# Performance work log

Measured on AMD Instinct MI355X. Metric: run time of the kernel, lower is better.

The kernel has to match this reference:

```python
import jax, jax.numpy as jnp
import numpy as np

B, N = 8, 50000
NB, NA, NT, NI, NC = 60000, 120000, 180000, 20000, 1500000


def _term_index(key, n_terms, arity, n_atoms):
    # distinct atom indices per term (avoids degenerate zero-length vectors)
    k1, k2 = jax.random.split(key)
    base = jax.random.randint(k1, (n_terms,), 0, n_atoms)
    cols = [base]
    for a in range(arity - 1):
        off = jax.random.randint(jax.random.fold_in(k2, a), (n_terms,), 1, n_atoms)
        cols.append((base + off + a) % n_atoms)
    return jnp.stack(cols, axis=1).astype(jnp.int32)


def setup_inputs() -> dict:
    key = jax.random.key(0)
    ks = jax.random.split(key, 24)
    u = lambda k, s, lo, hi: jax.random.uniform(k, s, jnp.float32, lo, hi)
    coords = jax.random.normal(ks[0], (B, N, 3), jnp.float32) * 10.0
    return dict(
        coords=coords,
        bond_index=_term_index(ks[1], NB, 2, N),
        bond_rest_length=u(ks[2], (NB,), 1.0, 2.0),
        bond_force_constant=u(ks[3], (NB,), 200.0, 800.0),
        angle_index=_term_index(ks[4], NA, 3, N),
        angle_force_constant=u(ks[5], (NA,), 50.0, 300.0),
        angle_c0=u(ks[6], (NA,), 0.5, 2.0),
        angle_c1=u(ks[7], (NA,), -1.0, 1.0),
        angle_c2=u(ks[8], (NA,), -1.0, 1.0),
        torsion_index=_term_index(ks[9], NT, 4, N),
        torsion_force_constant=u(ks[10], (NT,), 1.0, 20.0),
        torsion_order=jax.random.randint(ks[11], (NT,), 1, 7).astype(jnp.int32),
        torsion_cos_term=jnp.where(jax.random.bernoulli(ks[12], 0.5, (NT,)), 1.0, -1.0).astype(jnp.float32),
        inversion_index=_term_index(ks[13], NI, 4, N),
        inversion_force_constant=u(ks[14], (NI,), 1.0, 40.0),
        inversion_c0=u(ks[15], (NI,), 0.5, 1.5),
        inversion_c1=u(ks[16], (NI,), -1.0, 1.0),
        inversion_c2=u(ks[17], (NI,), -1.0, 1.0),
        nonbond_index=_term_index(ks[18], NC, 2, N),
        vdw_minimum=u(ks[19], (NC,), 3.0, 4.0),
        vdw_well_depth=u(ks[20], (NC,), 0.01, 0.2),
        vdw_threshold_sq=jnp.square(u(ks[21], (NC,), 10.0, 30.0)),
    )


def _uff_energy(coords, bond_index, bond_rest_length, bond_force_constant,
                angle_index, angle_force_constant, angle_c0, angle_c1, angle_c2,
                torsion_index, torsion_force_constant, torsion_order, torsion_cos_term,
                inversion_index, inversion_force_constant, inversion_c0, inversion_c1, inversion_c2,
                nonbond_index, vdw_minimum, vdw_well_depth, vdw_threshold_sq):
    take = lambda idx: jnp.take(coords, idx, axis=1)  # (B, P, 3)

    # ---- bond stretch: 0.5 * k * (|r_ij| - r0)^2 ----
    d = take(bond_index[:, 0]) - take(bond_index[:, 1])
    dist = jnp.sqrt(jnp.sum(d * d, -1))
    e_bond = jnp.sum(0.5 * bond_force_constant * jnp.square(dist - bond_rest_length), -1)

    # ---- angle bend (general cosine expansion, order == 0 branch) ----
    p1, p2, p3 = take(angle_index[:, 0]), take(angle_index[:, 1]), take(angle_index[:, 2])
    v1, v2 = p1 - p2, p3 - p2
    dot = jnp.sum(v1 * v2, -1)
    inv = jax.lax.rsqrt(jnp.maximum(jnp.sum(v1 * v1, -1) * jnp.sum(v2 * v2, -1), 1e-24))
    ct = jnp.clip(dot * inv, -0.999999, 0.999999)
    cs = ct * ct
    ss = jnp.maximum(1.0 - cs, 1e-12)
    e_angle = jnp.sum(angle_force_constant * (angle_c0 + angle_c1 * ct + angle_c2 * (cs - ss)), -1)

    # ---- torsion: 0.5 * V * (1 - cos_term * cos(n * phi)) ----
    q1, q2, q3, q4 = (take(torsion_index[:, a]) for a in range(4))
    b1, b2, b3 = q2 - q1, q3 - q2, q4 - q3
    n1 = jnp.cross(b1, b2)
    n2 = jnp.cross(b2, b3)
    cn = jnp.sum(n1 * n2, -1) * jax.lax.rsqrt(
        jnp.maximum(jnp.sum(n1 * n1, -1) * jnp.sum(n2 * n2, -1), 1e-24))
    phi = jnp.arccos(jnp.clip(cn, -0.999999, 0.999999))
    n_f = torsion_order.astype(coords.dtype)
    e_tor = jnp.sum(0.5 * torsion_force_constant * (1.0 - torsion_cos_term * jnp.cos(n_f * phi)), -1)

    # ---- inversion (Wilson angle): K*(c0 + c1*sinY + c2*(2*sinY^2 - 1)), central atom = col 1 ----
    cA = take(inversion_index[:, 1])
    rji = take(inversion_index[:, 0]) - cA
    rjk = take(inversion_index[:, 2]) - cA
    rjl = take(inversion_index[:, 3]) - cA
    nrm = jnp.cross(rji, rjk)
    cosY = jnp.sum(nrm * rjl, -1) * jax.lax.rsqrt(
        jnp.maximum(jnp.sum(nrm * nrm, -1) * jnp.sum(rjl * rjl, -1), 1e-24))
    cosY = jnp.clip(cosY, -0.999999, 0.999999)
    sinY = jnp.sqrt(jnp.maximum(1.0 - cosY * cosY, 0.0))
    e_inv = jnp.sum(inversion_force_constant * (inversion_c0 + inversion_c1 * sinY
                                                + inversion_c2 * (2.0 * sinY * sinY - 1.0)), -1)

    # ---- vdW LJ on radius-graph candidates: D*((R/r)^12 - 2*(R/r)^6) within cutoff ----
    dnb = take(nonbond_index[:, 0]) - take(nonbond_index[:, 1])
    d2 = jnp.sum(dnb * dnb, -1)
    within = d2 <= vdw_threshold_sq  # pair selection done under no_grad in the original
    x2 = jnp.square(vdw_minimum) / jnp.maximum(d2, 1e-12)
    x6 = x2 * x2 * x2
    e_pair = vdw_well_depth * (x6 * x6 - 2.0 * x6)
    e_vdw = jnp.sum(jnp.where(within, e_pair, 0.0), -1)

    return e_bond + e_angle + e_tor + e_inv + e_vdw  # (B,)


def reference(coords, bond_index, bond_rest_length, bond_force_constant,
              angle_index, angle_force_constant, angle_c0, angle_c1, angle_c2,
              torsion_index, torsion_force_constant, torsion_order, torsion_cos_term,
              inversion_index, inversion_force_constant, inversion_c0, inversion_c1, inversion_c2,
              nonbond_index, vdw_minimum, vdw_well_depth, vdw_threshold_sq):
    return _uff_energy(coords, bond_index, bond_rest_length, bond_force_constant,
                       angle_index, angle_force_constant, angle_c0, angle_c1, angle_c2,
                       torsion_index, torsion_force_constant, torsion_order, torsion_cos_term,
                       inversion_index, inversion_force_constant, inversion_c0, inversion_c1, inversion_c2,
                       nonbond_index, vdw_minimum, vdw_well_depth, vdw_threshold_sq)
```

## Files before the change

kernel.cpp:

```cpp
#include <hip/hip_runtime.h>

#define TPB 256
#define NWAVE (TPB / 64)
#define GRID_MAIN 2048

typedef int vi2 __attribute__((ext_vector_type(2)));
typedef int vi4 __attribute__((ext_vector_type(4)));

struct SegInfo {
    int e0, e1, e2, e3, e4;
    int NB, NA, NT, NI, NC;
    int N;
};

__device__ __forceinline__ float clamp1(float x) {
    return fminf(fmaxf(x, -0.999999f), 0.999999f);
}

__device__ __forceinline__ float ntf(const float* p) { return __builtin_nontemporal_load(p); }
__device__ __forceinline__ int   nti(const int* p)   { return __builtin_nontemporal_load(p); }

template <bool USE_WS>
__device__ __forceinline__ float4 loadC(const float4* __restrict__ cw,
                                        const float* __restrict__ coords,
                                        int N, int atom, int b) {
    if (USE_WS) {
        return cw[((size_t)atom << 3) + b];
    } else {
        const float* sp = coords + ((size_t)b * N + atom) * 3;
        return make_float4(sp[0], sp[1], sp[2], 0.f);
    }
}

__global__ void __launch_bounds__(TPB) transpose_coords(const float* __restrict__ coords,
                                                        float4* __restrict__ cw,
                                                        float* __restrict__ out, int N) {
    const int a = blockIdx.x * TPB + threadIdx.x;
    if (blockIdx.x == 0 && threadIdx.x < 8) out[threadIdx.x] = 0.f;
    if (a >= N) return;
#pragma unroll
    for (int b = 0; b < 8; b++) {
        const float* sp = coords + ((size_t)b * N + a) * 3;
        cw[((size_t)a << 3) + b] = make_float4(ntf(sp), ntf(sp + 1), ntf(sp + 2), 0.f);
    }
}

template <bool USE_WS>
__global__ void __launch_bounds__(TPB) uff_kernel(
    const float* __restrict__ coords, const float4* __restrict__ cw,
    const int* __restrict__ bidx, const float* __restrict__ br0, const float* __restrict__ bk,
    const int* __restrict__ aidx, const float* __restrict__ ak,
    const float* __restrict__ ac0, const float* __restrict__ ac1, const float* __restrict__ ac2,
    const int* __restrict__ tidx, const float* __restrict__ tk,
    const int* __restrict__ tord, const float* __restrict__ tcos,
    const int* __restrict__ iidx, const float* __restrict__ ik,
    const float* __restrict__ ic0, const float* __restrict__ ic1, const float* __restrict__ ic2,
    const int* __restrict__ nidx, const float* __restrict__ vmin,
    const float* __restrict__ vdep, const float* __restrict__ vthr,
    float* __restrict__ out, SegInfo s)
{
    const int tid = threadIdx.x;
    const int N = s.N;
    const int b = tid & 7;
    const int gidx = tid >> 3;
    float acc = 0.f;

    for (int c = blockIdx.x; c < s.e4; c += gridDim.x) {
        int kind, l;
        if (c < s.e0)      { kind = 0; l = c; }
        else if (c < s.e1) { kind = 1; l = c - s.e0; }
        else if (c < s.e2) { kind = 2; l = c - s.e1; }
        else if (c < s.e3) { kind = 3; l = c - s.e2; }
        else               { kind = 4; l = c - s.e3; }
        const int t = l * 32 + gidx;

        if (kind == 0) {
            if (t < s.NB) {
                const vi2 ij = __builtin_nontemporal_load((const vi2*)bidx + t);
                const float r0 = ntf(br0 + t), k = ntf(bk + t);
                float4 ci = loadC<USE_WS>(cw, coords, N, ij.x, b);
                float4 cj = loadC<USE_WS>(cw, coords, N, ij.y, b);
                float dx = ci.x - cj.x, dy = ci.y - cj.y, dz = ci.z - cj.z;
                float dd = sqrtf(dx * dx + dy * dy + dz * dz) - r0;
                acc += 0.5f * k * dd * dd;
            }
        } else if (kind == 1) {
            if (t < s.NA) {
                const int i1 = nti(aidx + 3 * t), i2 = nti(aidx + 3 * t + 1), i3 = nti(aidx + 3 * t + 2);
                const float k = ntf(ak + t), c0 = ntf(ac0 + t), c1 = ntf(ac1 + t), c2 = ntf(ac2 + t);
                float4 P = loadC<USE_WS>(cw, coords, N, i1, b);
                float4 Q = loadC<USE_WS>(cw, coords, N, i2, b);
                float4 R = loadC<USE_WS>(cw, coords, N, i3, b);
                float ax = P.x - Q.x, ay = P.y - Q.y, az = P.z - Q.z;
                float bx = R.x - Q.x, by = R.y - Q.y, bz = R.z - Q.z;
                float dot = ax * bx + ay * by + az * bz;
                float nn = (ax * ax + ay * ay + az * az) * (bx * bx + by * by + bz * bz);
                float ct = clamp1(dot * rsqrtf(fmaxf(nn, 1e-24f)));
                float cs = ct * ct;
                float sb = fmaxf(1.f - cs, 1e-12f);
                acc += k * (c0 + c1 * ct + c2 * (cs - sb));
            }
        } else if (kind == 2) {
            if (t < s.NT) {
                const vi4 q = __builtin_nontemporal_load((const vi4*)tidx + t);
                const float V = ntf(tk + t), ctm = ntf(tcos + t);
                const int ord = nti(tord + t);
                float4 P1 = loadC<USE_WS>(cw, coords, N, q.x, b);
                float4 P2 = loadC<USE_WS>(cw, coords, N, q.y, b);
                float4 P3 = loadC<USE_WS>(cw, coords, N, q.z, b);
                float4 P4 = loadC<USE_WS>(cw, coords, N, q.w, b);
                float b1x = P2.x - P1.x, b1y = P2.y - P1.y, b1z = P2.z - P1.z;
                float b2x = P3.x - P2.x, b2y = P3.y - P2.y, b2z = P3.z - P2.z;
                float b3x = P4.x - P3.x, b3y = P4.y - P3.y, b3z = P4.z - P3.z;
                float n1x = b1y * b2z - b1z * b2y;
                float n1y = b1z * b2x - b1x * b2z;
                float n1z = b1x * b2y - b1y * b2x;
                float n2x = b2y * b3z - b2z * b3y;
                float n2y = b2z * b3x - b2x * b3z;
                float n2z = b2x * b3y - b2y * b3x;
                float dot = n1x * n2x + n1y * n2y + n1z * n2z;
                float nn = (n1x * n1x + n1y * n1y + n1z * n1z) *
                           (n2x * n2x + n2y * n2y + n2z * n2z);
                float x = clamp1(dot * rsqrtf(fmaxf(nn, 1e-24f)));
                float Tp = 1.f, Tc = x, res = x;
#pragma unroll
                for (int kk = 2; kk <= 6; kk++) {
                    float Tn = 2.f * x * Tc - Tp;
                    Tp = Tc; Tc = Tn;
                    if (ord == kk) res = Tn;
                }
                acc += 0.5f * V * (1.f - ctm * res);
            }
        } else if (kind == 3) {
            if (t < s.NI) {
                const vi4 q = __builtin_nontemporal_load((const vi4*)iidx + t);
                const float K = ntf(ik + t), c0 = ntf(ic0 + t), c1 = ntf(ic1 + t), c2 = ntf(ic2 + t);
                float4 CA = loadC<USE_WS>(cw, coords, N, q.y, b);
                float4 PI = loadC<USE_WS>(cw, coords, N, q.x, b);
                float4 PK = loadC<USE_WS>(cw, coords, N, q.z, b);
                float4 PL = loadC<USE_WS>(cw, coords, N, q.w, b);
                float jix = PI.x - CA.x, jiy = PI.y - CA.y, jiz = PI.z - CA.z;
                float jkx = PK.x - CA.x, jky = PK.y - CA.y, jkz = PK.z - CA.z;
                float lx  = PL.x - CA.x, ly  = PL.y - CA.y, lz  = PL.z - CA.z;
                float nx = jiy * jkz - jiz * jky;
                float ny = jiz * jkx - jix * jkz;
                float nz = jix * jky - jiy * jkx;
                float dot = nx * lx + ny * ly + nz * lz;
                float nn = (nx * nx + ny * ny + nz * nz) * (lx * lx + ly * ly + lz * lz);
                float cosY = clamp1(dot * rsqrtf(fmaxf(nn, 1e-24f)));
                float sinY = sqrtf(fmaxf(1.f - cosY * cosY, 0.f));
                acc += K * (c0 + c1 * sinY + c2 * (2.f * sinY * sinY - 1.f));
            }
        } else {
            if (t < s.NC) {
                const vi2 ij = __builtin_nontemporal_load((const vi2*)nidx + t);
                const float R = ntf(vmin + t), D = ntf(vdep + t), thr = ntf(vthr + t);
                float4 ci = loadC<USE_WS>(cw, coords, N, ij.x, b);
                float4 cj = loadC<USE_WS>(cw, coords, N, ij.y, b);
                float dx = ci.x - cj.x, dy = ci.y - cj.y, dz = ci.z - cj.z;
                float d2 = dx * dx + dy * dy + dz * dz;
                float x2 = (R * R) / fmaxf(d2, 1e-12f);
                float x6 = x2 * x2 * x2;
                float e = D * (x6 * x6 - 2.f * x6);
                if (d2 <= thr) acc += e;
            }
        }
    }

    float v = acc;
    v += __shfl_down(v, 8, 64);
    v += __shfl_down(v, 16, 64);
    v += __shfl_down(v, 32, 64);

    __shared__ float red[NWAVE][8];
    const int lane = tid & 63;
    const int wid = tid >> 6;
    if (lane < 8) red[wid][lane] = v;
    __syncthreads();
    if (tid < 8) {
        float ssum = 0.f;
#pragma unroll
        for (int w = 0; w < NWAVE; w++) ssum += red[w][tid];
        atomicAdd(&out[tid], ssum);
    }
}

static inline int cdiv(int a, int b) { return (a + b - 1) / b; }

extern "C" void kernel_launch(void* const* d_in, const int* in_sizes, int n_in,
                              void* d_out, int out_size, void* d_ws, size_t ws_size,
                              hipStream_t stream) {
    const int B = out_size;
    const int NB = in_sizes[2], NA = in_sizes[5], NT = in_sizes[10],
              NI = in_sizes[14], NC = in_sizes[19];
    const int N = in_sizes[0] / (3 * B);

    const float* coords = (const float*)d_in[0];
    const int*   bidx = (const int*)d_in[1];
    const float* br0  = (const float*)d_in[2];
    const float* bk   = (const float*)d_in[3];
    const int*   aidx = (const int*)d_in[4];
    const float* ak   = (const float*)d_in[5];
    const float* ac0  = (const float*)d_in[6];
    const float* ac1  = (const float*)d_in[7];
    const float* ac2  = (const float*)d_in[8];
    const int*   tidx = (const int*)d_in[9];
    const float* tk   = (const float*)d_in[10];
    const int*   tord = (const int*)d_in[11];
    const float* tcos = (const float*)d_in[12];
    const int*   iidx = (const int*)d_in[13];
    const float* ik   = (const float*)d_in[14];
    const float* ic0  = (const float*)d_in[15];
    const float* ic1  = (const float*)d_in[16];
    const float* ic2  = (const float*)d_in[17];
    const int*   nidx = (const int*)d_in[18];
    const float* vmin = (const float*)d_in[19];
    const float* vdep = (const float*)d_in[20];
    const float* vthr = (const float*)d_in[21];

    const size_t ws_need = (size_t)N * 8 * sizeof(float4);
    const bool use_ws = ws_size >= ws_need;
    float4* cw = (float4*)d_ws;

    if (use_ws) {
        transpose_coords<<<cdiv(N, TPB), TPB, 0, stream>>>(coords, cw, (float*)d_out, N);
    } else {
        hipMemsetAsync(d_out, 0, (size_t)out_size * sizeof(float), stream);
    }

    SegInfo s;
    s.NB = NB; s.NA = NA; s.NT = NT; s.NI = NI; s.NC = NC; s.N = N;
    s.e0 = cdiv(NB, 32);
    s.e1 = s.e0 + cdiv(NA, 32);
    s.e2 = s.e1 + cdiv(NT, 32);
    s.e3 = s.e2 + cdiv(NI, 32);
    s.e4 = s.e3 + cdiv(NC, 32);

    const int grid = (s.e4 < GRID_MAIN) ? s.e4 : GRID_MAIN;

    if (use_ws) {
        uff_kernel<true><<<grid, TPB, 0, stream>>>(
            coords, cw, bidx, br0, bk, aidx, ak, ac0, ac1, ac2,
            tidx, tk, tord, tcos, iidx, ik, ic0, ic1, ic2,
            nidx, vmin, vdep, vthr, (float*)d_out, s);
    } else {
        uff_kernel<false><<<grid, TPB, 0, stream>>>(
            coords, cw, bidx, br0, bk, aidx, ak, ac0, ac1, ac2,
            tidx, tk, tord, tcos, iidx, ik, ic0, ic1, ic2,
            nidx, vmin, vdep, vthr, (float*)d_out, s);
    }
}
```

Before: 199.3 us.

## Split per-term-type loops, broadcast term params via shuffle, double up LJ pairs

Replaces the single grid-stride loop with its per-chunk kind dispatch by five separate grid-stride loops, one per term type. Within each group of 8 lanes, only lane 0 now loads the term indices and parameters, and the values reach the other 7 lanes through wavefront shuffles. This removes the eightfold redundant per-batch loads of the same term data. The nonbond loop handles two pairs per lane group per iteration to expose more memory-level parallelism, at the cost of extra shuffle instructions and a serialized dependency on lane 0's load.

```diff
diff --git a/kernel.cpp b/kernel.cpp
--- a/kernel.cpp
+++ b/kernel.cpp
@@ -8,7 +8,7 @@
 typedef int vi4 __attribute__((ext_vector_type(4)));
 
 struct SegInfo {
-    int e0, e1, e2, e3, e4;
+    int cb, ca, ct, ci, cl;
     int NB, NA, NT, NI, NC;
     int N;
 };
@@ -18,7 +18,9 @@
 }
 
 __device__ __forceinline__ float ntf(const float* p) { return __builtin_nontemporal_load(p); }
-__device__ __forceinline__ int   nti(const int* p)   { return __builtin_nontemporal_load(p); }
+
+__device__ __forceinline__ float bcf(float v, int sl) { return __shfl(v, sl, 64); }
+__device__ __forceinline__ int   bci(int v, int sl)   { return __shfl(v, sl, 64); }
 
 template <bool USE_WS>
 __device__ __forceinline__ float4 loadC(const float4* __restrict__ cw,
@@ -60,110 +62,159 @@
     float* __restrict__ out, SegInfo s)
 {
     const int tid = threadIdx.x;
+    const int lane = tid & 63;
+    const int b = tid & 7;
+    const int g = tid >> 3;
+    const int sl = lane & ~7;
     const int N = s.N;
-    const int b = tid & 7;
-    const int gidx = tid >> 3;
     float acc = 0.f;
 
-    for (int c = blockIdx.x; c < s.e4; c += gridDim.x) {
-        int kind, l;
-        if (c < s.e0)      { kind = 0; l = c; }
-        else if (c < s.e1) { kind = 1; l = c - s.e0; }
-        else if (c < s.e2) { kind = 2; l = c - s.e1; }
-        else if (c < s.e3) { kind = 3; l = c - s.e2; }
-        else               { kind = 4; l = c - s.e3; }
-        const int t = l * 32 + gidx;
-
-        if (kind == 0) {
-            if (t < s.NB) {
-                const vi2 ij = __builtin_nontemporal_load((const vi2*)bidx + t);
-                const float r0 = ntf(br0 + t), k = ntf(bk + t);
-                float4 ci = loadC<USE_WS>(cw, coords, N, ij.x, b);
-                float4 cj = loadC<USE_WS>(cw, coords, N, ij.y, b);
-                float dx = ci.x - cj.x, dy = ci.y - cj.y, dz = ci.z - cj.z;
-                float dd = sqrtf(dx * dx + dy * dy + dz * dz) - r0;
-                acc += 0.5f * k * dd * dd;
-            }
-        } else if (kind == 1) {
-            if (t < s.NA) {
-                const int i1 = nti(aidx + 3 * t), i2 = nti(aidx + 3 * t + 1), i3 = nti(aidx + 3 * t + 2);
-                const float k = ntf(ak + t), c0 = ntf(ac0 + t), c1 = ntf(ac1 + t), c2 = ntf(ac2 + t);
-                float4 P = loadC<USE_WS>(cw, coords, N, i1, b);
-                float4 Q = loadC<USE_WS>(cw, coords, N, i2, b);
-                float4 R = loadC<USE_WS>(cw, coords, N, i3, b);
-                float ax = P.x - Q.x, ay = P.y - Q.y, az = P.z - Q.z;
-                float bx = R.x - Q.x, by = R.y - Q.y, bz = R.z - Q.z;
-                float dot = ax * bx + ay * by + az * bz;
-                float nn = (ax * ax + ay * ay + az * az) * (bx * bx + by * by + bz * bz);
-                float ct = clamp1(dot * rsqrtf(fmaxf(nn, 1e-24f)));
-                float cs = ct * ct;
-                float sb = fmaxf(1.f - cs, 1e-12f);
-                acc += k * (c0 + c1 * ct + c2 * (cs - sb));
-            }
-        } else if (kind == 2) {
-            if (t < s.NT) {
-                const vi4 q = __builtin_nontemporal_load((const vi4*)tidx + t);
-                const float V = ntf(tk + t), ctm = ntf(tcos + t);
-                const int ord = nti(tord + t);
-                float4 P1 = loadC<USE_WS>(cw, coords, N, q.x, b);
-                float4 P2 = loadC<USE_WS>(cw, coords, N, q.y, b);
-                float4 P3 = loadC<USE_WS>(cw, coords, N, q.z, b);
-                float4 P4 = loadC<USE_WS>(cw, coords, N, q.w, b);
-                float b1x = P2.x - P1.x, b1y = P2.y - P1.y, b1z = P2.z - P1.z;
-                float b2x = P3.x - P2.x, b2y = P3.y - P2.y, b2z = P3.z - P2.z;
-                float b3x = P4.x - P3.x, b3y = P4.y - P3.y, b3z = P4.z - P3.z;
-                float n1x = b1y * b2z - b1z * b2y;
-                float n1y = b1z * b2x - b1x * b2z;
-                float n1z = b1x * b2y - b1y * b2x;
-                float n2x = b2y * b3z - b2z * b3y;
-                float n2y = b2z * b3x - b2x * b3z;
-                float n2z = b2x * b3y - b2y * b3x;
-                float dot = n1x * n2x + n1y * n2y + n1z * n2z;
-                float nn = (n1x * n1x + n1y * n1y + n1z * n1z) *
-                           (n2x * n2x + n2y * n2y + n2z * n2z);
-                float x = clamp1(dot * rsqrtf(fmaxf(nn, 1e-24f)));
-                float Tp = 1.f, Tc = x, res = x;
+    for (int c = blockIdx.x; c < s.cb; c += gridDim.x) {
+        const int t = c * 32 + g;
+        const bool ok = t < s.NB;
+        int ijx = 0, ijy = 0; float r0 = 0.f, k = 0.f;
+        if (ok && b == 0) {
+            const vi2 ij = __builtin_nontemporal_load((const vi2*)bidx + t);
+            ijx = ij.x; ijy = ij.y; r0 = ntf(br0 + t); k = ntf(bk + t);
+        }
+        ijx = bci(ijx, sl); ijy = bci(ijy, sl); r0 = bcf(r0, sl); k = bcf(k, sl);
+        float4 ci = loadC<USE_WS>(cw, coords, N, ijx, b);
+        float4 cj = loadC<USE_WS>(cw, coords, N, ijy, b);
+        float dx = ci.x - cj.x, dy = ci.y - cj.y, dz = ci.z - cj.z;
+        float dd = sqrtf(dx * dx + dy * dy + dz * dz) - r0;
+        if (ok) acc += 0.5f * k * dd * dd;
+    }
+
+    for (int c = blockIdx.x; c < s.ca; c += gridDim.x) {
+        const int t = c * 32 + g;
+        const bool ok = t < s.NA;
+        int i1 = 0, i2 = 0, i3 = 0; float k = 0.f, c0 = 0.f, c1 = 0.f, c2 = 0.f;
+        if (ok && b == 0) {
+            i1 = aidx[3 * t]; i2 = aidx[3 * t + 1]; i3 = aidx[3 * t + 2];
+            k = ntf(ak + t); c0 = ntf(ac0 + t); c1 = ntf(ac1 + t); c2 = ntf(ac2 + t);
+        }
+        i1 = bci(i1, sl); i2 = bci(i2, sl); i3 = bci(i3, sl);
+        k = bcf(k, sl); c0 = bcf(c0, sl); c1 = bcf(c1, sl); c2 = bcf(c2, sl);
+        float4 P = loadC<USE_WS>(cw, coords, N, i1, b);
+        float4 Q = loadC<USE_WS>(cw, coords, N, i2, b);
+        float4 R = loadC<USE_WS>(cw, coords, N, i3, b);
+        float ax = P.x - Q.x, ay = P.y - Q.y, az = P.z - Q.z;
+        float bx = R.x - Q.x, by = R.y - Q.y, bz = R.z - Q.z;
+        float dot = ax * bx + ay * by + az * bz;
+        float nn = (ax * ax + ay * ay + az * az) * (bx * bx + by * by + bz * bz);
+        float ct = clamp1(dot * rsqrtf(fmaxf(nn, 1e-24f)));
+        float cs = ct * ct;
+        float sb = fmaxf(1.f - cs, 1e-12f);
+        if (ok) acc += k * (c0 + c1 * ct + c2 * (cs - sb));
+    }
+
+    for (int c = blockIdx.x; c < s.ct; c += gridDim.x) {
+        const int t = c * 32 + g;
+        const bool ok = t < s.NT;
+        int q0 = 0, q1 = 0, q2 = 0, q3 = 0, ord = 1;
+        float V = 0.f, ctm = 0.f;
+        if (ok && b == 0) {
+            const vi4 q = __builtin_nontemporal_load((const vi4*)tidx + t);
+            q0 = q.x; q1 = q.y; q2 = q.z; q3 = q.w;
+            V = ntf(tk + t); ctm = ntf(tcos + t);
+            ord = __builtin_nontemporal_load(tord + t);
+        }
+        q0 = bci(q0, sl); q1 = bci(q1, sl); q2 = bci(q2, sl); q3 = bci(q3, sl);
+        V = bcf(V, sl); ctm = bcf(ctm, sl); ord = bci(ord, sl);
+        float4 P1 = loadC<USE_WS>(cw, coords, N, q0, b);
+        float4 P2 = loadC<USE_WS>(cw, coords, N, q1, b);
+        float4 P3 = loadC<USE_WS>(cw, coords, N, q2, b);
+        float4 P4 = loadC<USE_WS>(cw, coords, N, q3, b);
+        float b1x = P2.x - P1.x, b1y = P2.y - P1.y, b1z = P2.z - P1.z;
+        float b2x = P3.x - P2.x, b2y = P3.y - P2.y, b2z = P3.z - P2.z;
+        float b3x = P4.x - P3.x, b3y = P4.y - P3.y, b3z = P4.z - P3.z;
+        float n1x = b1y * b2z - b1z * b2y;
+        float n1y = b1z * b2x - b1x * b2z;
+        float n1z = b1x * b2y - b1y * b2x;
+        float n2x = b2y * b3z - b2z * b3y;
+        float n2y = b2z * b3x - b2x * b3z;
+        float n2z = b2x * b3y - b2y * b3x;
+        float dot = n1x * n2x + n1y * n2y + n1z * n2z;
+        float nn = (n1x * n1x + n1y * n1y + n1z * n1z) *
+                   (n2x * n2x + n2y * n2y + n2z * n2z);
+        float x = clamp1(dot * rsqrtf(fmaxf(nn, 1e-24f)));
+        float Tp = 1.f, Tc = x, res = x;
 #pragma unroll
-                for (int kk = 2; kk <= 6; kk++) {
-                    float Tn = 2.f * x * Tc - Tp;
-                    Tp = Tc; Tc = Tn;
-                    if (ord == kk) res = Tn;
-                }
-                acc += 0.5f * V * (1.f - ctm * res);
-            }
-        } else if (kind == 3) {
-            if (t < s.NI) {
-                const vi4 q = __builtin_nontemporal_load((const vi4*)iidx + t);
-                const float K = ntf(ik + t), c0 = ntf(ic0 + t), c1 = ntf(ic1 + t), c2 = ntf(ic2 + t);
-                float4 CA = loadC<USE_WS>(cw, coords, N, q.y, b);
-                float4 PI = loadC<USE_WS>(cw, coords, N, q.x, b);
-                float4 PK = loadC<USE_WS>(cw, coords, N, q.z, b);
-                float4 PL = loadC<USE_WS>(cw, coords, N, q.w, b);
-                float jix = PI.x - CA.x, jiy = PI.y - CA.y, jiz = PI.z - CA.z;
-                float jkx = PK.x - CA.x, jky = PK.y - CA.y, jkz = PK.z - CA.z;
-                float lx  = PL.x - CA.x, ly  = PL.y - CA.y, lz  = PL.z - CA.z;
-                float nx = jiy * jkz - jiz * jky;
-                float ny = jiz * jkx - jix * jkz;
-                float nz = jix * jky - jiy * jkx;
-                float dot = nx * lx + ny * ly + nz * lz;
-                float nn = (nx * nx + ny * ny + nz * nz) * (lx * lx + ly * ly + lz * lz);
-                float cosY = clamp1(dot * rsqrtf(fmaxf(nn, 1e-24f)));
-                float sinY = sqrtf(fmaxf(1.f - cosY * cosY, 0.f));
-                acc += K * (c0 + c1 * sinY + c2 * (2.f * sinY * sinY - 1.f));
-            }
-        } else {
-            if (t < s.NC) {
-                const vi2 ij = __builtin_nontemporal_load((const vi2*)nidx + t);
-                const float R = ntf(vmin + t), D = ntf(vdep + t), thr = ntf(vthr + t);
-                float4 ci = loadC<USE_WS>(cw, coords, N, ij.x, b);
-                float4 cj = loadC<USE_WS>(cw, coords, N, ij.y, b);
-                float dx = ci.x - cj.x, dy = ci.y - cj.y, dz = ci.z - cj.z;
-                float d2 = dx * dx + dy * dy + dz * dz;
-                float x2 = (R * R) / fmaxf(d2, 1e-12f);
-                float x6 = x2 * x2 * x2;
-                float e = D * (x6 * x6 - 2.f * x6);
-                if (d2 <= thr) acc += e;
-            }
+        for (int kk = 2; kk <= 6; kk++) {
+            float Tn = 2.f * x * Tc - Tp;
+            Tp = Tc; Tc = Tn;
+            if (ord == kk) res = Tn;
+        }
+        if (ok) acc += 0.5f * V * (1.f - ctm * res);
+    }
+
+    for (int c = blockIdx.x; c < s.ci; c += gridDim.x) {
+        const int t = c * 32 + g;
+        const bool ok = t < s.NI;
+        int q0 = 0, q1 = 0, q2 = 0, q3 = 0;
+        float K = 0.f, c0 = 0.f, c1 = 0.f, c2 = 0.f;
+        if (ok && b == 0) {
+            const vi4 q = __builtin_nontemporal_load((const vi4*)iidx + t);
+            q0 = q.x; q1 = q.y; q2 = q.z; q3 = q.w;
+            K = ntf(ik + t); c0 = ntf(ic0 + t); c1 = ntf(ic1 + t); c2 = ntf(ic2 + t);
+        }
+        q0 = bci(q0, sl); q1 = bci(q1, sl); q2 = bci(q2, sl); q3 = bci(q3, sl);
+        K = bcf(K, sl); c0 = bcf(c0, sl); c1 = bcf(c1, sl); c2 = bcf(c2, sl);
+        float4 CA = loadC<USE_WS>(cw, coords, N, q1, b);
+        float4 PI = loadC<USE_WS>(cw, coords, N, q0, b);
+        float4 PK = loadC<USE_WS>(cw, coords, N, q2, b);
+        float4 PL = loadC<USE_WS>(cw, coords, N, q3, b);
+        float jix = PI.x - CA.x, jiy = PI.y - CA.y, jiz = PI.z - CA.z;
+        float jkx = PK.x - CA.x, jky = PK.y - CA.y, jkz = PK.z - CA.z;
+        float lx  = PL.x - CA.x, ly  = PL.y - CA.y, lz  = PL.z - CA.z;
+        float nx = jiy * jkz - jiz * jky;
+        float ny = jiz * jkx - jix * jkz;
+        float nz = jix * jky - jiy * jkx;
+        float dot = nx * lx + ny * ly + nz * lz;
+        float nn = (nx * nx + ny * ny + nz * nz) * (lx * lx + ly * ly + lz * lz);
+        float cosY = clamp1(dot * rsqrtf(fmaxf(nn, 1e-24f)));
+        float sinY = sqrtf(fmaxf(1.f - cosY * cosY, 0.f));
+        if (ok) acc += K * (c0 + c1 * sinY + c2 * (2.f * sinY * sinY - 1.f));
+    }
+
+    for (int c = blockIdx.x; c < s.cl; c += gridDim.x) {
+        const int t0 = c * 64 + g;
+        const int t1 = t0 + 32;
+        const bool ok0 = t0 < s.NC, ok1 = t1 < s.NC;
+        int ax0 = 0, ay0 = 0, ax1 = 0, ay1 = 0;
+        float R0 = 0.f, D0 = 0.f, th0 = 0.f, R1 = 0.f, D1 = 0.f, th1 = 0.f;
+        if (ok0 && b == 0) {
+            const vi2 ij = __builtin_nontemporal_load((const vi2*)nidx + t0);
+            ax0 = ij.x; ay0 = ij.y;
+            R0 = ntf(vmin + t0); D0 = ntf(vdep + t0); th0 = ntf(vthr + t0);
+        }
+        if (ok1 && b == 0) {
+            const vi2 ij = __builtin_nontemporal_load((const vi2*)nidx + t1);
+            ax1 = ij.x; ay1 = ij.y;
+            R1 = ntf(vmin + t1); D1 = ntf(vdep + t1); th1 = ntf(vthr + t1);
+        }
+        ax0 = bci(ax0, sl); ay0 = bci(ay0, sl); ax1 = bci(ax1, sl); ay1 = bci(ay1, sl);
+        R0 = bcf(R0, sl); D0 = bcf(D0, sl); th0 = bcf(th0, sl);
+        R1 = bcf(R1, sl); D1 = bcf(D1, sl); th1 = bcf(th1, sl);
+        float4 ci0 = loadC<USE_WS>(cw, coords, N, ax0, b);
+        float4 cj0 = loadC<USE_WS>(cw, coords, N, ay0, b);
+        float4 ci1 = loadC<USE_WS>(cw, coords, N, ax1, b);
+        float4 cj1 = loadC<USE_WS>(cw, coords, N, ay1, b);
+        {
+            float dx = ci0.x - cj0.x, dy = ci0.y - cj0.y, dz = ci0.z - cj0.z;
+            float d2 = dx * dx + dy * dy + dz * dz;
+            float x2 = (R0 * R0) / fmaxf(d2, 1e-12f);
+            float x6 = x2 * x2 * x2;
+            float e = D0 * (x6 * x6 - 2.f * x6);
+            if (ok0 && d2 <= th0) acc += e;
+        }
+        {
+            float dx = ci1.x - cj1.x, dy = ci1.y - cj1.y, dz = ci1.z - cj1.z;
+            float d2 = dx * dx + dy * dy + dz * dz;
+            float x2 = (R1 * R1) / fmaxf(d2, 1e-12f);
+            float x6 = x2 * x2 * x2;
+            float e = D1 * (x6 * x6 - 2.f * x6);
+            if (ok1 && d2 <= th1) acc += e;
         }
     }
 
@@ -173,7 +224,6 @@
     v += __shfl_down(v, 32, 64);
 
     __shared__ float red[NWAVE][8];
-    const int lane = tid & 63;
     const int wid = tid >> 6;
     if (lane < 8) red[wid][lane] = v;
     __syncthreads();
@@ -230,21 +280,19 @@
 
     SegInfo s;
     s.NB = NB; s.NA = NA; s.NT = NT; s.NI = NI; s.NC = NC; s.N = N;
-    s.e0 = cdiv(NB, 32);
-    s.e1 = s.e0 + cdiv(NA, 32);
-    s.e2 = s.e1 + cdiv(NT, 32);
-    s.e3 = s.e2 + cdiv(NI, 32);
-    s.e4 = s.e3 + cdiv(NC, 32);
-
-    const int grid = (s.e4 < GRID_MAIN) ? s.e4 : GRID_MAIN;
+    s.cb = cdiv(NB, 32);
+    s.ca = cdiv(NA, 32);
+    s.ct = cdiv(NT, 32);
+    s.ci = cdiv(NI, 32);
+    s.cl = cdiv(NC, 64);
 
     if (use_ws) {
-        uff_kernel<true><<<grid, TPB, 0, stream>>>(
+        uff_kernel<true><<<GRID_MAIN, TPB, 0, stream>>>(
             coords, cw, bidx, br0, bk, aidx, ak, ac0, ac1, ac2,
             tidx, tk, tord, tcos, iidx, ik, ic0, ic1, ic2,
             nidx, vmin, vdep, vthr, (float*)d_out, s);
     } else {
-        uff_kernel<false><<<grid, TPB, 0, stream>>>(
+        uff_kernel<false><<<GRID_MAIN, TPB, 0, stream>>>(
             coords, cw, bidx, br0, bk, aidx, ak, ac0, ac1, ac2,
             tidx, tk, tord, tcos, iidx, ik, ic0, ic1, ic2,
             nidx, vmin, vdep, vthr, (float*)d_out, s);
```

New measurement: 177.8 us. 10.8% less time.

## Stage term params in LDS per 256-term chunk, split into per-kind loops

Applied to the files above, without the earlier changes.

Replaces the single grid-stride loop with its per-chunk kind dispatch by five separate grid-stride loops, one per term type. In each, a block cooperatively loads 256 terms' indices and parameters with one coalesced load per thread into shared memory, then 8-lane groups process 8 terms each. This avoids the old pattern where all 8 batch lanes re-read the same index and parameter words, and removes the per-chunk branching. It adds two barriers per chunk, and the grid is now fixed at 2048 blocks regardless of the amount of work.

```diff
diff --git a/kernel.cpp b/kernel.cpp
--- a/kernel.cpp
+++ b/kernel.cpp
@@ -2,13 +2,14 @@
 
 #define TPB 256
 #define NWAVE (TPB / 64)
+#define CHUNK 256
 #define GRID_MAIN 2048
 
 typedef int vi2 __attribute__((ext_vector_type(2)));
 typedef int vi4 __attribute__((ext_vector_type(4)));
 
 struct SegInfo {
-    int e0, e1, e2, e3, e4;
+    int cb, ca, ct, ci, cl;
     int NB, NA, NT, NI, NC;
     int N;
 };
@@ -18,7 +19,6 @@
 }
 
 __device__ __forceinline__ float ntf(const float* p) { return __builtin_nontemporal_load(p); }
-__device__ __forceinline__ int   nti(const int* p)   { return __builtin_nontemporal_load(p); }
 
 template <bool USE_WS>
 __device__ __forceinline__ float4 loadC(const float4* __restrict__ cw,
@@ -59,112 +59,182 @@
     const float* __restrict__ vdep, const float* __restrict__ vthr,
     float* __restrict__ out, SegInfo s)
 {
+    __shared__ int4   sI[CHUNK];
+    __shared__ float4 sP[CHUNK];
+
     const int tid = threadIdx.x;
+    const int lane = tid & 63;
+    const int b = tid & 7;
+    const int g = tid >> 3;
     const int N = s.N;
-    const int b = tid & 7;
-    const int gidx = tid >> 3;
     float acc = 0.f;
 
-    for (int c = blockIdx.x; c < s.e4; c += gridDim.x) {
-        int kind, l;
-        if (c < s.e0)      { kind = 0; l = c; }
-        else if (c < s.e1) { kind = 1; l = c - s.e0; }
-        else if (c < s.e2) { kind = 2; l = c - s.e1; }
-        else if (c < s.e3) { kind = 3; l = c - s.e2; }
-        else               { kind = 4; l = c - s.e3; }
-        const int t = l * 32 + gidx;
-
-        if (kind == 0) {
-            if (t < s.NB) {
-                const vi2 ij = __builtin_nontemporal_load((const vi2*)bidx + t);
-                const float r0 = ntf(br0 + t), k = ntf(bk + t);
-                float4 ci = loadC<USE_WS>(cw, coords, N, ij.x, b);
-                float4 cj = loadC<USE_WS>(cw, coords, N, ij.y, b);
-                float dx = ci.x - cj.x, dy = ci.y - cj.y, dz = ci.z - cj.z;
-                float dd = sqrtf(dx * dx + dy * dy + dz * dz) - r0;
-                acc += 0.5f * k * dd * dd;
+    for (int c = blockIdx.x; c < s.cb; c += gridDim.x) {
+        const int base = c * CHUNK;
+        {
+            const int u = min(base + tid, s.NB - 1);
+            const vi2 ij = __builtin_nontemporal_load((const vi2*)bidx + u);
+            sI[tid] = make_int4(ij.x, ij.y, 0, 0);
+            sP[tid] = make_float4(ntf(br0 + u), ntf(bk + u), 0.f, 0.f);
+        }
+        __syncthreads();
+#pragma unroll 2
+        for (int j = 0; j < 8; j++) {
+            const int slot = g + 32 * j;
+            const int4 q = sI[slot];
+            const float4 p = sP[slot];
+            float4 ci = loadC<USE_WS>(cw, coords, N, q.x, b);
+            float4 cj = loadC<USE_WS>(cw, coords, N, q.y, b);
+            float dx = ci.x - cj.x, dy = ci.y - cj.y, dz = ci.z - cj.z;
+            float dd = sqrtf(dx * dx + dy * dy + dz * dz) - p.x;
+            if (base + slot < s.NB) acc += 0.5f * p.y * dd * dd;
+        }
+        __syncthreads();
+    }
+
+    for (int c = blockIdx.x; c < s.ca; c += gridDim.x) {
+        const int base = c * CHUNK;
+        {
+            const int u = min(base + tid, s.NA - 1);
+            sI[tid] = make_int4(aidx[3 * u], aidx[3 * u + 1], aidx[3 * u + 2], 0);
+            sP[tid] = make_float4(ntf(ak + u), ntf(ac0 + u), ntf(ac1 + u), ntf(ac2 + u));
+        }
+        __syncthreads();
+#pragma unroll 2
+        for (int j = 0; j < 8; j++) {
+            const int slot = g + 32 * j;
+            const int4 q = sI[slot];
+            const float4 p = sP[slot];
+            float4 P = loadC<USE_WS>(cw, coords, N, q.x, b);
+            float4 Q = loadC<USE_WS>(cw, coords, N, q.y, b);
+            float4 R = loadC<USE_WS>(cw, coords, N, q.z, b);
+            float ax = P.x - Q.x, ay = P.y - Q.y, az = P.z - Q.z;
+            float bx = R.x - Q.x, by = R.y - Q.y, bz = R.z - Q.z;
+            float dot = ax * bx + ay * by + az * bz;
+            float nn = (ax * ax + ay * ay + az * az) * (bx * bx + by * by + bz * bz);
+            float ct = clamp1(dot * rsqrtf(fmaxf(nn, 1e-24f)));
+            float cs = ct * ct;
+            float sb = fmaxf(1.f - cs, 1e-12f);
+            if (base + slot < s.NA) acc += p.x * (p.y + p.z * ct + p.w * (cs - sb));
+        }
+        __syncthreads();
+    }
+
+    for (int c = blockIdx.x; c < s.ct; c += gridDim.x) {
+        const int base = c * CHUNK;
+        {
+            const int u = min(base + tid, s.NT - 1);
+            const vi4 q = __builtin_nontemporal_load((const vi4*)tidx + u);
+            sI[tid] = make_int4(q.x, q.y, q.z, q.w);
+            sP[tid] = make_float4(ntf(tk + u), ntf(tcos + u),
+                                  __int_as_float(__builtin_nontemporal_load(tord + u)), 0.f);
+        }
+        __syncthreads();
+#pragma unroll 2
+        for (int j = 0; j < 8; j++) {
+            const int slot = g + 32 * j;
+            const int4 q = sI[slot];
+            const float4 p = sP[slot];
+            const int ord = __float_as_int(p.z);
+            float4 P1 = loadC<USE_WS>(cw, coords, N, q.x, b);
+            float4 P2 = loadC<USE_WS>(cw, coords, N, q.y, b);
+            float4 P3 = loadC<USE_WS>(cw, coords, N, q.z, b);
+            float4 P4 = loadC<USE_WS>(cw, coords, N, q.w, b);
+            float b1x = P2.x - P1.x, b1y = P2.y - P1.y, b1z = P2.z - P1.z;
+            float b2x = P3.x - P2.x, b2y = P3.y - P2.y, b2z = P3.z - P2.z;
+            float b3x = P4.x - P3.x, b3y = P4.y - P3.y, b3z = P4.z - P3.z;
+            float n1x = b1y * b2z - b1z * b2y;
+            float n1y = b1z * b2x - b1x * b2z;
+            float n1z = b1x * b2y - b1y * b2x;
+            float n2x = b2y * b3z - b2z * b3y;
+            float n2y = b2z * b3x - b2x * b3z;
+            float n2z = b2x * b3y - b2y * b3x;
+            float dot = n1x * n2x + n1y * n2y + n1z * n2z;
+            float nn = (n1x * n1x + n1y * n1y + n1z * n1z) *
+                       (n2x * n2x + n2y * n2y + n2z * n2z);
+            float x = clamp1(dot * rsqrtf(fmaxf(nn, 1e-24f)));
+            float Tp = 1.f, Tc = x, res = x;
+#pragma unroll
+            for (int kk = 2; kk <= 6; kk++) {
+                float Tn = 2.f * x * Tc - Tp;
+                Tp = Tc; Tc = Tn;
+                if (ord == kk) res = Tn;
             }
-        } else if (kind == 1) {
-            if (t < s.NA) {
-                const int i1 = nti(aidx + 3 * t), i2 = nti(aidx + 3 * t + 1), i3 = nti(aidx + 3 * t + 2);
-                const float k = ntf(ak + t), c0 = ntf(ac0 + t), c1 = ntf(ac1 + t), c2 = ntf(ac2 + t);
-                float4 P = loadC<USE_WS>(cw, coords, N, i1, b);
-                float4 Q = loadC<USE_WS>(cw, coords, N, i2, b);
-                float4 R = loadC<USE_WS>(cw, coords, N, i3, b);
-                float ax = P.x - Q.x, ay = P.y - Q.y, az = P.z - Q.z;
-                float bx = R.x - Q.x, by = R.y - Q.y, bz = R.z - Q.z;
-                float dot = ax * bx + ay * by + az * bz;
-                float nn = (ax * ax + ay * ay + az * az) * (bx * bx + by * by + bz * bz);
-                float ct = clamp1(dot * rsqrtf(fmaxf(nn, 1e-24f)));
-                float cs = ct * ct;
-                float sb = fmaxf(1.f - cs, 1e-12f);
-                acc += k * (c0 + c1 * ct + c2 * (cs - sb));
+            if (base + slot < s.NT) acc += 0.5f * p.x * (1.f - p.y * res);
+        }
+        __syncthreads();
+    }
+
+    for (int c = blockIdx.x; c < s.ci; c += gridDim.x) {
+        const int base = c * CHUNK;
+        {
+            const int u = min(base + tid, s.NI - 1);
+            const vi4 q = __builtin_nontemporal_load((const vi4*)iidx + u);
+            sI[tid] = make_int4(q.x, q.y, q.z, q.w);
+            sP[tid] = make_float4(ntf(ik + u), ntf(ic0 + u), ntf(ic1 + u), ntf(ic2 + u));
+        }
+        __syncthreads();
+#pragma unroll 2
+        for (int j = 0; j < 8; j++) {
+            const int slot = g + 32 * j;
+            const int4 q = sI[slot];
+            const float4 p = sP[slot];
+            float4 CA = loadC<USE_WS>(cw, coords, N, q.y, b);
+            float4 PI = loadC<USE_WS>(cw, coords, N, q.x, b);
+            float4 PK = loadC<USE_WS>(cw, coords, N, q.z, b);
+            float4 PL = loadC<USE_WS>(cw, coords, N, q.w, b);
+            float jix = PI.x - CA.x, jiy = PI.y - CA.y, jiz = PI.z - CA.z;
+            float jkx = PK.x - CA.x, jky = PK.y - CA.y, jkz = PK.z - CA.z;
+            float lx  = PL.x - CA.x, ly  = PL.y - CA.y, lz  = PL.z - CA.z;
+            float nx = jiy * jkz - jiz * jky;
+            float ny = jiz * jkx - jix * jkz;
+            float nz = jix * jky - jiy * jkx;
+            float dot = nx * lx + ny * ly + nz * lz;
+            float nn = (nx * nx + ny * ny + nz * nz) * (lx * lx + ly * ly + lz * lz);
+            float cosY = clamp1(dot * rsqrtf(fmaxf(nn, 1e-24f)));
+            float sinY = sqrtf(fmaxf(1.f - cosY * cosY, 0.f));
+            if (base + slot < s.NI) acc += p.x * (p.y + p.z * sinY + p.w * (2.f * sinY * sinY - 1.f));
+        }
+        __syncthreads();
+    }
+
+    for (int c = blockIdx.x; c < s.cl; c += gridDim.x) {
+        const int base = c * CHUNK;
+        {
+            const int u = min(base + tid, s.NC - 1);
+            const vi2 ij = __builtin_nontemporal_load((const vi2*)nidx + u);
+            const float R = ntf(vmin + u);
+            sI[tid] = make_int4(ij.x, ij.y, 0, 0);
+            sP[tid] = make_float4(R * R, ntf(vdep + u), ntf(vthr + u), 0.f);
+        }
+        __syncthreads();
+#pragma unroll
+        for (int j = 0; j < 8; j += 2) {
+            const int s0 = g + 32 * j, s1 = s0 + 32;
+            const int4 q0 = sI[s0]; const float4 p0 = sP[s0];
+            const int4 q1 = sI[s1]; const float4 p1 = sP[s1];
+            float4 a0 = loadC<USE_WS>(cw, coords, N, q0.x, b);
+            float4 b0 = loadC<USE_WS>(cw, coords, N, q0.y, b);
+            float4 a1 = loadC<USE_WS>(cw, coords, N, q1.x, b);
+            float4 b1 = loadC<USE_WS>(cw, coords, N, q1.y, b);
+            {
+                float dx = a0.x - b0.x, dy = a0.y - b0.y, dz = a0.z - b0.z;
+                float d2 = dx * dx + dy * dy + dz * dz;
+                float x2 = p0.x / fmaxf(d2, 1e-12f);
+                float x6 = x2 * x2 * x2;
+                float e = p0.y * (x6 * x6 - 2.f * x6);
+                if (base + s0 < s.NC && d2 <= p0.z) acc += e;
             }
-        } else if (kind == 2) {
-            if (t < s.NT) {
-                const vi4 q = __builtin_nontemporal_load((const vi4*)tidx + t);
-                const float V = ntf(tk + t), ctm = ntf(tcos + t);
-                const int ord = nti(tord + t);
-                float4 P1 = loadC<USE_WS>(cw, coords, N, q.x, b);
-                float4 P2 = loadC<USE_WS>(cw, coords, N, q.y, b);
-                float4 P3 = loadC<USE_WS>(cw, coords, N, q.z, b);
-                float4 P4 = loadC<USE_WS>(cw, coords, N, q.w, b);
-                float b1x = P2.x - P1.x, b1y = P2.y - P1.y, b1z = P2.z - P1.z;
-                float b2x = P3.x - P2.x, b2y = P3.y - P2.y, b2z = P3.z - P2.z;
-                float b3x = P4.x - P3.x, b3y = P4.y - P3.y, b3z = P4.z - P3.z;
-                float n1x = b1y * b2z - b1z * b2y;
-                float n1y = b1z * b2x - b1x * b2z;
-                float n1z = b1x * b2y - b1y * b2x;
-                float n2x = b2y * b3z - b2z * b3y;
-                float n2y = b2z * b3x - b2x * b3z;
-                float n2z = b2x * b3y - b2y * b3x;
-                float dot = n1x * n2x + n1y * n2y + n1z * n2z;
-                float nn = (n1x * n1x + n1y * n1y + n1z * n1z) *
-                           (n2x * n2x + n2y * n2y + n2z * n2z);
-                float x = clamp1(dot * rsqrtf(fmaxf(nn, 1e-24f)));
-                float Tp = 1.f, Tc = x, res = x;
-#pragma unroll
-                for (int kk = 2; kk <= 6; kk++) {
-                    float Tn = 2.f * x * Tc - Tp;
-                    Tp = Tc; Tc = Tn;
-                    if (ord == kk) res = Tn;
-                }
-                acc += 0.5f * V * (1.f - ctm * res);
+            {
+                float dx = a1.x - b1.x, dy = a1.y - b1.y, dz = a1.z - b1.z;
+                float d2 = dx * dx + dy * dy + dz * dz;
+                float x2 = p1.x / fmaxf(d2, 1e-12f);
+                float x6 = x2 * x2 * x2;
+                float e = p1.y * (x6 * x6 - 2.f * x6);
+                if (base + s1 < s.NC && d2 <= p1.z) acc += e;
             }
-        } else if (kind == 3) {
-            if (t < s.NI) {
-                const vi4 q = __builtin_nontemporal_load((const vi4*)iidx + t);
-                const float K = ntf(ik + t), c0 = ntf(ic0 + t), c1 = ntf(ic1 + t), c2 = ntf(ic2 + t);
-                float4 CA = loadC<USE_WS>(cw, coords, N, q.y, b);
-                float4 PI = loadC<USE_WS>(cw, coords, N, q.x, b);
-                float4 PK = loadC<USE_WS>(cw, coords, N, q.z, b);
-                float4 PL = loadC<USE_WS>(cw, coords, N, q.w, b);
-                float jix = PI.x - CA.x, jiy = PI.y - CA.y, jiz = PI.z - CA.z;
-                float jkx = PK.x - CA.x, jky = PK.y - CA.y, jkz = PK.z - CA.z;
-                float lx  = PL.x - CA.x, ly  = PL.y - CA.y, lz  = PL.z - CA.z;
-                float nx = jiy * jkz - jiz * jky;
-                float ny = jiz * jkx - jix * jkz;
-                float nz = jix * jky - jiy * jkx;
-                float dot = nx * lx + ny * ly + nz * lz;
-                float nn = (nx * nx + ny * ny + nz * nz) * (lx * lx + ly * ly + lz * lz);
-                float cosY = clamp1(dot * rsqrtf(fmaxf(nn, 1e-24f)));
-                float sinY = sqrtf(fmaxf(1.f - cosY * cosY, 0.f));
-                acc += K * (c0 + c1 * sinY + c2 * (2.f * sinY * sinY - 1.f));
-            }
-        } else {
-            if (t < s.NC) {
-                const vi2 ij = __builtin_nontemporal_load((const vi2*)nidx + t);
-                const float R = ntf(vmin + t), D = ntf(vdep + t), thr = ntf(vthr + t);
-                float4 ci = loadC<USE_WS>(cw, coords, N, ij.x, b);
-                float4 cj = loadC<USE_WS>(cw, coords, N, ij.y, b);
-                float dx = ci.x - cj.x, dy = ci.y - cj.y, dz = ci.z - cj.z;
-                float d2 = dx * dx + dy * dy + dz * dz;
-                float x2 = (R * R) / fmaxf(d2, 1e-12f);
-                float x6 = x2 * x2 * x2;
-                float e = D * (x6 * x6 - 2.f * x6);
-                if (d2 <= thr) acc += e;
-            }
-        }
+        }
+        __syncthreads();
     }
 
     float v = acc;
@@ -173,7 +243,6 @@
     v += __shfl_down(v, 32, 64);
 
     __shared__ float red[NWAVE][8];
-    const int lane = tid & 63;
     const int wid = tid >> 6;
     if (lane < 8) red[wid][lane] = v;
     __syncthreads();
@@ -230,21 +299,19 @@
 
     SegInfo s;
     s.NB = NB; s.NA = NA; s.NT = NT; s.NI = NI; s.NC = NC; s.N = N;
-    s.e0 = cdiv(NB, 32);
-    s.e1 = s.e0 + cdiv(NA, 32);
-    s.e2 = s.e1 + cdiv(NT, 32);
-    s.e3 = s.e2 + cdiv(NI, 32);
-    s.e4 = s.e3 + cdiv(NC, 32);
-
-    const int grid = (s.e4 < GRID_MAIN) ? s.e4 : GRID_MAIN;
+    s.cb = cdiv(NB, CHUNK);
+    s.ca = cdiv(NA, CHUNK);
+    s.ct = cdiv(NT, CHUNK);
+    s.ci = cdiv(NI, CHUNK);
+    s.cl = cdiv(NC, CHUNK);
 
     if (use_ws) {
-        uff_kernel<true><<<grid, TPB, 0, stream>>>(
+        uff_kernel<true><<<GRID_MAIN, TPB, 0, stream>>>(
             coords, cw, bidx, br0, bk, aidx, ak, ac0, ac1, ac2,
             tidx, tk, tord, tcos, iidx, ik, ic0, ic1, ic2,
             nidx, vmin, vdep, vthr, (float*)d_out, s);
     } else {
-        uff_kernel<false><<<grid, TPB, 0, stream>>>(
+        uff_kernel<false><<<GRID_MAIN, TPB, 0, stream>>>(
             coords, cw, bidx, br0, bk, aidx, ak, ac0, ac1, ac2,
             tidx, tk, tord, tcos, iidx, ik, ic0, ic1, ic2,
             nidx, vmin, vdep, vthr, (float*)d_out, s);
```

Result: faster. 168.8 us (-15.3%).
